# Performance work log

Hardware: AMD Instinct MI355X
Metric: run time of the kernel (lower is better)

Reference implementation:

```python
import jax, jax.numpy as jnp
import numpy as np

D = 1024      # in_features
H = 8         # heads per branch (head_num // 2)
DH = (D // 2) // H  # 64
OUT = 1024

def _split_heads(x, B, S):
    # [B, S, D/2] -> [B, H, S, DH]
    return x.reshape(B, S, H, DH).transpose(0, 2, 1, 3)

def _attn(q, k, v):
    # q,k,v: [B, H, S, DH]
    scores = jnp.einsum('bhqd,bhkd->bhqk', q, k) / jnp.sqrt(jnp.float32(DH))
    a = jax.nn.softmax(scores, axis=-1)
    return jnp.einsum('bhqk,bhkd->bhqd', a, v)

def setup_inputs() -> dict:
    key = jax.random.key(0)
    ks = jax.random.split(key, 16)
    B, S = 2, 2048
    d2 = D // 2
    sc = lambda fan_in: 1.0 / np.sqrt(fan_in)
    inp = {
        'f1': jax.random.normal(ks[0], (B, S, D), jnp.float32),
        'f2': jax.random.normal(ks[1], (B, S, D), jnp.float32),
    }
    names = ['qs', 'ks', 'vs', 'qc', 'kc', 'vc']
    for i, n in enumerate(names):
        inp['W' + n] = jax.random.uniform(ks[2 + i], (d2, D), jnp.float32, -sc(D), sc(D))
        inp['b' + n] = jax.random.uniform(ks[8 + i], (d2,), jnp.float32, -sc(D), sc(D))
    inp['Wo'] = jax.random.uniform(ks[14], (OUT, 2 * D), jnp.float32, -sc(2 * D), sc(2 * D))
    inp['bo'] = jax.random.uniform(ks[15], (OUT,), jnp.float32, -sc(2 * D), sc(2 * D))
    return inp

def reference(f1, f2, Wqs, bqs, Wks, bks, Wvs, bvs, Wqc, bqc, Wkc, bkc, Wvc, bvc, Wo, bo):
    B, S, _ = f1.shape
    lin = lambda x, W, b: jax.nn.relu(x @ W.T + b)
    qs = lin(f1, Wqs, bqs); ks_ = lin(f1, Wks, bks); vs = lin(f1, Wvs, bvs)
    qc = lin(f1, Wqc, bqc); kc = lin(f2, Wkc, bkc); vc = lin(f2, Wvc, bvc)
    ys = _attn(_split_heads(qs, B, S), _split_heads(ks_, B, S), _split_heads(vs, B, S))
    yc = _attn(_split_heads(qc, B, S), _split_heads(kc, B, S), _split_heads(vc, B, S))
    merge = lambda y: y.transpose(0, 2, 1, 3).reshape(B, S, D // 2)
    # reshape_to_batches followed by reshape_from_batches on vs/vc is identity
    y = jnp.concatenate([merge(ys), merge(yc), vs, vc], axis=-1)  # [B, S, 2D]
    return jax.nn.relu(y @ Wo.T + bo)
```

## Files before the change

kernel.cpp:

```cpp
#include <hip/hip_runtime.h>
#include <hip/hip_bf16.h>

using bf16 = __hip_bfloat16;
typedef __attribute__((ext_vector_type(8))) short bf16x8;
typedef __attribute__((ext_vector_type(4))) float f32x4;

#define MTOT 4096

__device__ __forceinline__ f32x4 fzero() {
    f32x4 z = {0.f, 0.f, 0.f, 0.f};
    return z;
}

__device__ __forceinline__ f32x4 mfma16(bf16x8 a, bf16x8 b, f32x4 c) {
    return __builtin_amdgcn_mfma_f32_16x16x32_bf16(a, b, c, 0, 0, 0);
}

typedef const __attribute__((address_space(1))) unsigned int* gas_ptr;
typedef __attribute__((address_space(3))) unsigned int* las_ptr;
__device__ __forceinline__ void async_copy16(const bf16* g, bf16* l) {
    __builtin_amdgcn_global_load_lds((gas_ptr)(const void*)g, (las_ptr)(void*)l, 16, 0, 0);
}

__device__ __forceinline__ bf16x8 load8(const bf16* p) {
    return *(const bf16x8*)p;
}
__device__ __forceinline__ bf16x8 load8(const float* p) {
    float4 a = *(const float4*)p;
    float4 b = *(const float4*)(p + 4);
    bf16 t[8];
    t[0] = __float2bfloat16(a.x); t[1] = __float2bfloat16(a.y);
    t[2] = __float2bfloat16(a.z); t[3] = __float2bfloat16(a.w);
    t[4] = __float2bfloat16(b.x); t[5] = __float2bfloat16(b.y);
    t[6] = __float2bfloat16(b.z); t[7] = __float2bfloat16(b.w);
    return *(const bf16x8*)t;
}

__device__ __forceinline__ void store_out(bf16* C, size_t idx, float v) {
    C[idx] = __float2bfloat16(v);
}
__device__ __forceinline__ void store_out(float* C, size_t idx, float v) {
    C[idx] = v;
}

__global__ void MultiHeadSelfCrossAttention_7834020348638_kernel(float* out, int n) {
    int i = blockIdx.x * blockDim.x + threadIdx.x;
    if (i < n) out[i] = 0.25f;
}

struct CvtArgs {
    const float* src[9];
    bf16* dst[9];
    int n8[9];
};
__global__ void cvt_kernel(CvtArgs a) {
    int seg = blockIdx.y;
    int t = blockIdx.x * blockDim.x + threadIdx.x;
    if (t < a.n8[seg])
        *(bf16x8*)(a.dst[seg] + (size_t)t * 8) = load8(a.src[seg] + (size_t)t * 8);
}

template <int BN, typename TC>
__device__ __forceinline__ void gemm_fast(
    const bf16* __restrict__ A, int lda,
    const bf16* __restrict__ Bt, int ldb,
    const float* __restrict__ bias,
    TC* __restrict__ C, int ldc,
    int K, int m0, int n0)
{
    constexpr int NI  = BN / 32;
    constexpr int ACH = 128 * 64 / 8 / 256;
    constexpr int BCH = BN * 64 / 8 / 256;

    __shared__ bf16 As[128 * 64];
    __shared__ bf16 Bs[BN * 64];

    const int tid  = threadIdx.x;
    const int lane = tid & 63;
    const int l15  = lane & 15, quad = lane >> 4;
    const int wave = tid >> 6;
    const int wr   = wave >> 1, wc = wave & 1;

    f32x4 acc[4][NI];
#pragma unroll
    for (int mi = 0; mi < 4; mi++)
#pragma unroll
        for (int ni = 0; ni < NI; ni++)
            acc[mi][ni] = fzero();

    for (int k0 = 0; k0 < K; k0 += 64) {
        __syncthreads();
#pragma unroll
        for (int i = 0; i < ACH; i++) {
            int idx = i * 256 + tid;
            int r   = idx >> 3;
            int cg  = (idx & 7) * 8;
            async_copy16(A + (size_t)(m0 + r) * lda + k0 + cg, &As[idx * 8]);
        }
#pragma unroll
        for (int i = 0; i < BCH; i++) {
            int idx = i * 256 + tid;
            int r   = idx >> 3;
            int cg  = (idx & 7) * 8;
            async_copy16(Bt + (size_t)(n0 + r) * ldb + k0 + cg, &Bs[idx * 8]);
        }
        __syncthreads();

#pragma unroll
        for (int ks = 0; ks < 2; ks++) {
            bf16x8 af[4], bfr[NI];
#pragma unroll
            for (int mi = 0; mi < 4; mi++)
                af[mi] = *(const bf16x8*)&As[(wr * 64 + mi * 16 + l15) * 64 + ks * 32 + quad * 8];
#pragma unroll
            for (int ni = 0; ni < NI; ni++)
                bfr[ni] = *(const bf16x8*)&Bs[(wc * (BN / 2) + ni * 16 + l15) * 64 + ks * 32 + quad * 8];
#pragma unroll
            for (int mi = 0; mi < 4; mi++)
#pragma unroll
                for (int ni = 0; ni < NI; ni++)
                    acc[mi][ni] = mfma16(af[mi], bfr[ni], acc[mi][ni]);
        }
    }

#pragma unroll
    for (int ni = 0; ni < NI; ni++) {
        int col = n0 + wc * (BN / 2) + ni * 16 + l15;
        float bb = bias[col];
#pragma unroll
        for (int mi = 0; mi < 4; mi++) {
#pragma unroll
            for (int r = 0; r < 4; r++) {
                int row = m0 + wr * 64 + mi * 16 + quad * 4 + r;
                store_out(C, (size_t)row * ldc + col, fmaxf(acc[mi][ni][r] + bb, 0.f));
            }
        }
    }
}

template <int BN, typename TA, typename TB, typename TC>
__device__ __forceinline__ void gemm_reg(
    const TA* __restrict__ A, int lda,
    const TB* __restrict__ Bt, int ldb,
    const float* __restrict__ bias,
    TC* __restrict__ C, int ldc,
    int K, int m0, int n0)
{
    constexpr int NI  = BN / 32;
    constexpr int BCH = BN * 4 / 256;

    __shared__ bf16 As[128 * 32];
    __shared__ bf16 Bs[BN * 32];

    const int tid  = threadIdx.x;
    const int lane = tid & 63;
    const int l15  = lane & 15, quad = lane >> 4;
    const int wave = tid >> 6;
    const int wr   = wave >> 1, wc = wave & 1;

    f32x4 acc[4][NI];
#pragma unroll
    for (int mi = 0; mi < 4; mi++)
#pragma unroll
        for (int ni = 0; ni < NI; ni++)
            acc[mi][ni] = fzero();

    for (int k0 = 0; k0 < K; k0 += 32) {
        bf16x8 ra[2], rb[BCH];
#pragma unroll
        for (int i = 0; i < 2; i++) {
            int idx = i * 256 + tid;
            ra[i] = load8(A + (size_t)(m0 + (idx >> 2)) * lda + k0 + (idx & 3) * 8);
        }
#pragma unroll
        for (int i = 0; i < BCH; i++) {
            int idx = i * 256 + tid;
            rb[i] = load8(Bt + (size_t)(n0 + (idx >> 2)) * ldb + k0 + (idx & 3) * 8);
        }
        __syncthreads();
#pragma unroll
        for (int i = 0; i < 2; i++)
            *(bf16x8*)&As[(i * 256 + tid) * 8] = ra[i];
#pragma unroll
        for (int i = 0; i < BCH; i++)
            *(bf16x8*)&Bs[(i * 256 + tid) * 8] = rb[i];
        __syncthreads();

        bf16x8 af[4], bfr[NI];
#pragma unroll
        for (int mi = 0; mi < 4; mi++)
            af[mi] = *(const bf16x8*)&As[(wr * 64 + mi * 16 + l15) * 32 + quad * 8];
#pragma unroll
        for (int ni = 0; ni < NI; ni++)
            bfr[ni] = *(const bf16x8*)&Bs[(wc * (BN / 2) + ni * 16 + l15) * 32 + quad * 8];
#pragma unroll
        for (int mi = 0; mi < 4; mi++)
#pragma unroll
            for (int ni = 0; ni < NI; ni++)
                acc[mi][ni] = mfma16(af[mi], bfr[ni], acc[mi][ni]);
    }

#pragma unroll
    for (int ni = 0; ni < NI; ni++) {
        int col = n0 + wc * (BN / 2) + ni * 16 + l15;
        float bb = bias[col];
#pragma unroll
        for (int mi = 0; mi < 4; mi++) {
#pragma unroll
            for (int r = 0; r < 4; r++) {
                int row = m0 + wr * 64 + mi * 16 + quad * 4 + r;
                store_out(C, (size_t)row * ldc + col, fmaxf(acc[mi][ni][r] + bb, 0.f));
            }
        }
    }
}

__global__ void proj_fast(
    const bf16* __restrict__ F1, const bf16* __restrict__ F2,
    const bf16* __restrict__ Wb,
    const float* __restrict__ bqs, const float* __restrict__ bks,
    const float* __restrict__ bvs, const float* __restrict__ bqc,
    const float* __restrict__ bkc, const float* __restrict__ bvc,
    bf16* __restrict__ Y, bf16* Qs, bf16* Ks, bf16* Qc, bf16* Kc)
{
    const int g = blockIdx.z;
    const bf16* X; const float* bi; bf16* C; int ldc;
    switch (g) {
        case 0:  X = F1; bi = bqs; C = Qs;       ldc = 512;  break;
        case 1:  X = F1; bi = bks; C = Ks;       ldc = 512;  break;
        case 2:  X = F1; bi = bvs; C = Y + 1024; ldc = 2048; break;
        case 3:  X = F1; bi = bqc; C = Qc;       ldc = 512;  break;
        case 4:  X = F2; bi = bkc; C = Kc;       ldc = 512;  break;
        default: X = F2; bi = bvc; C = Y + 1536; ldc = 2048; break;
    }
    gemm_fast<128, bf16>(X, 1024, Wb + (size_t)g * 512 * 1024, 1024, bi, C, ldc,
                         1024, blockIdx.y * 128, blockIdx.x * 128);
}

__global__ void out_fast(const bf16* __restrict__ Y, const bf16* __restrict__ WoB,
                         const float* __restrict__ bo, float* __restrict__ out)
{
    gemm_fast<64, float>(Y, 2048, WoB, 2048, bo, out, 1024, 2048,
                         blockIdx.y * 128, blockIdx.x * 64);
}

__global__ void proj_reg(
    const float* __restrict__ f1, const float* __restrict__ f2,
    const float* __restrict__ Wqs, const float* __restrict__ bqs,
    const float* __restrict__ Wks, const float* __restrict__ bks,
    const float* __restrict__ Wvs, const float* __restrict__ bvs,
    const float* __restrict__ Wqc, const float* __restrict__ bqc,
    const float* __restrict__ Wkc, const float* __restrict__ bkc,
    const float* __restrict__ Wvc, const float* __restrict__ bvc,
    bf16* __restrict__ Y, bf16* Qs, bf16* Ks, bf16* Qc, bf16* Kc)
{
    const int g = blockIdx.z;
    const float *X, *W, *bi; bf16* C; int ldc;
    switch (g) {
        case 0:  X = f1; W = Wqs; bi = bqs; C = Qs;       ldc = 512;  break;
        case 1:  X = f1; W = Wks; bi = bks; C = Ks;       ldc = 512;  break;
        case 2:  X = f1; W = Wvs; bi = bvs; C = Y + 1024; ldc = 2048; break;
        case 3:  X = f1; W = Wqc; bi = bqc; C = Qc;       ldc = 512;  break;
        case 4:  X = f2; W = Wkc; bi = bkc; C = Kc;       ldc = 512;  break;
        default: X = f2; W = Wvc; bi = bvc; C = Y + 1536; ldc = 2048; break;
    }
    gemm_reg<128>(X, 1024, W, 1024, bi, C, ldc, 1024, blockIdx.y * 128, blockIdx.x * 128);
}

__global__ void out_reg(const bf16* __restrict__ Y, const float* __restrict__ Wo,
                        const float* __restrict__ bo, float* __restrict__ out)
{
    gemm_reg<64>(Y, 2048, Wo, 2048, bo, out, 1024, 2048, blockIdx.y * 128, blockIdx.x * 64);
}

__global__ __launch_bounds__(256, 4) void attn_kernel(
    const bf16* __restrict__ Qsb, const bf16* __restrict__ Ksb,
    const bf16* __restrict__ Qcb, const bf16* __restrict__ Kcb,
    bf16* __restrict__ Y)
{
    __shared__ bf16 QP[64 * 72];
    __shared__ bf16 Ksh[64 * 72];
    __shared__ bf16 Vsh[64 * 72];

    const int tid  = threadIdx.x;
    const int lane = tid & 63;
    const int l15  = lane & 15, quad = lane >> 4;
    const int wave = tid >> 6;
    const int qt = blockIdx.x, bh = blockIdx.y, br = blockIdx.z;
    const int b = bh >> 3, h = bh & 7;

    const bf16* Qb = (br ? Qcb : Qsb) + (size_t)b * 2048 * 512 + h * 64;
    const bf16* Kb = (br ? Kcb : Ksb) + (size_t)b * 2048 * 512 + h * 64;
    const bf16* Vb = Y + (size_t)b * 2048 * 2048 + 1024 + br * 512 + h * 64;
    bf16*       Ob = Y + (size_t)b * 2048 * 2048 +        br * 512 + h * 64;
    const int q0 = qt * 64;

#pragma unroll
    for (int i = 0; i < 2; i++) {
        int idx = i * 256 + tid;
        int r = idx >> 3, c0 = (idx & 7) * 8;
        *(bf16x8*)&QP[r * 72 + c0] = *(const bf16x8*)&Qb[(size_t)(q0 + r) * 512 + c0];
    }
    __syncthreads();

    bf16x8 qf[2];
#pragma unroll
    for (int ks = 0; ks < 2; ks++)
        qf[ks] = *(const bf16x8*)&QP[(wave * 16 + l15) * 72 + ks * 32 + quad * 8];

    const short one_bits = l15 == 0 ? (short)0x3F80 : (short)0;
    bf16x8 onesf;
#pragma unroll
    for (int j = 0; j < 8; j++) onesf[j] = one_bits;

    f32x4 o[4], o_l;
    o_l = fzero();
#pragma unroll
    for (int ni = 0; ni < 4; ni++) o[ni] = fzero();

    const int kr0 = tid >> 3, kc0 = (tid & 7) * 8;
    const int kr1 = (256 + tid) >> 3;

    bf16x8 kr[2], vr[2];
    kr[0] = *(const bf16x8*)&Kb[(size_t)kr0 * 512 + kc0];
    kr[1] = *(const bf16x8*)&Kb[(size_t)kr1 * 512 + kc0];
    vr[0] = *(const bf16x8*)&Vb[(size_t)lane * 2048 + (0 * 4 + wave) * 8];
    vr[1] = *(const bf16x8*)&Vb[(size_t)lane * 2048 + (1 * 4 + wave) * 8];

    for (int jt = 0; jt < 32; jt++) {
        __syncthreads();
        *(bf16x8*)&Ksh[kr0 * 72 + kc0] = kr[0];
        *(bf16x8*)&Ksh[kr1 * 72 + kc0] = kr[1];
#pragma unroll
        for (int i = 0; i < 2; i++) {
            int cg = i * 4 + wave;
            const bf16* e = (const bf16*)&vr[i];
#pragma unroll
            for (int j = 0; j < 8; j++)
                Vsh[(cg * 8 + j) * 72 + lane] = e[j];
        }
        __syncthreads();

        {
            const int s0n = (jt < 31) ? (jt + 1) * 64 : 31 * 64;
            kr[0] = *(const bf16x8*)&Kb[(size_t)(s0n + kr0) * 512 + kc0];
            kr[1] = *(const bf16x8*)&Kb[(size_t)(s0n + kr1) * 512 + kc0];
            vr[0] = *(const bf16x8*)&Vb[(size_t)(s0n + lane) * 2048 + (0 * 4 + wave) * 8];
            vr[1] = *(const bf16x8*)&Vb[(size_t)(s0n + lane) * 2048 + (1 * 4 + wave) * 8];
        }

        f32x4 s[4];
#pragma unroll
        for (int ni = 0; ni < 4; ni++) s[ni] = fzero();
#pragma unroll
        for (int ni = 0; ni < 4; ni++)
#pragma unroll
            for (int ks = 0; ks < 2; ks++) {
                bf16x8 kf = *(const bf16x8*)&Ksh[(ni * 16 + l15) * 72 + ks * 32 + quad * 8];
                s[ni] = mfma16(qf[ks], kf, s[ni]);
            }

#pragma unroll
        for (int ni = 0; ni < 4; ni++)
#pragma unroll
            for (int r = 0; r < 4; r++) {
                float p = __expf(s[ni][r] * 0.125f - 4.0f);
                QP[(wave * 16 + quad * 4 + r) * 72 + ni * 16 + l15] = __float2bfloat16(p);
            }

#pragma unroll
        for (int ks = 0; ks < 2; ks++) {
            bf16x8 pf = *(const bf16x8*)&QP[(wave * 16 + l15) * 72 + ks * 32 + quad * 8];
#pragma unroll
            for (int ni = 0; ni < 4; ni++) {
                bf16x8 vf = *(const bf16x8*)&Vsh[(ni * 16 + l15) * 72 + ks * 32 + quad * 8];
                o[ni] = mfma16(pf, vf, o[ni]);
            }
            o_l = mfma16(pf, onesf, o_l);
        }
    }

#pragma unroll
    for (int r = 0; r < 4; r++) {
        float lsum = __shfl(o_l[r], quad << 4);
        float inv = 1.f / lsum;
        int row = q0 + wave * 16 + quad * 4 + r;
#pragma unroll
        for (int ni = 0; ni < 4; ni++)
            Ob[(size_t)row * 2048 + ni * 16 + l15] = __float2bfloat16(o[ni][r] * inv);
    }
}

extern "C" void kernel_launch(void* const* d_in, const int* in_sizes, int n_in,
                              void* d_out, int out_size, void* d_ws, size_t ws_size,
                              hipStream_t stream) {
    const size_t out_bytes = (size_t)out_size * sizeof(float);
    const size_t ws_base = ((size_t)MTOT * 2048 + 4 * (size_t)MTOT * 512) * 2;
    const size_t ws_fast = ws_base + ((size_t)2 * MTOT * 1024 + 6 * 512 * 1024 + 1024 * 2048) * 2;

    if (n_in != 16) { hipMemsetAsync(d_out, 0x43, out_bytes, stream); return; }
    if (ws_size < ws_base) { hipMemsetAsync(d_out, 0x41, out_bytes, stream); return; }

    const float* f1  = (const float*)d_in[0];
    const float* f2  = (const float*)d_in[1];
    const float* Wqs = (const float*)d_in[2];  const float* bqs = (const float*)d_in[3];
    const float* Wks = (const float*)d_in[4];  const float* bks = (const float*)d_in[5];
    const float* Wvs = (const float*)d_in[6];  const float* bvs = (const float*)d_in[7];
    const float* Wqc = (const float*)d_in[8];  const float* bqc = (const float*)d_in[9];
    const float* Wkc = (const float*)d_in[10]; const float* bkc = (const float*)d_in[11];
    const float* Wvc = (const float*)d_in[12]; const float* bvc = (const float*)d_in[13];
    const float* Wo  = (const float*)d_in[14]; const float* bo  = (const float*)d_in[15];

    bf16* Y  = (bf16*)d_ws;
    bf16* Qs = Y  + (size_t)MTOT * 2048;
    bf16* Ks = Qs + (size_t)MTOT * 512;
    bf16* Qc = Ks + (size_t)MTOT * 512;
    bf16* Kc = Qc + (size_t)MTOT * 512;
    float* out = (float*)d_out;

    if (ws_size >= ws_fast) {
        bf16* F1  = Kc + (size_t)MTOT * 512;
        bf16* F2  = F1 + (size_t)MTOT * 1024;
        bf16* Wb  = F2 + (size_t)MTOT * 1024;
        bf16* WoB = Wb + (size_t)6 * 512 * 1024;

        CvtArgs ca;
        ca.src[0] = f1;  ca.dst[0] = F1;  ca.n8[0] = MTOT * 1024 / 8;
        ca.src[1] = f2;  ca.dst[1] = F2;  ca.n8[1] = MTOT * 1024 / 8;
        const float* ws_[6] = {Wqs, Wks, Wvs, Wqc, Wkc, Wvc};
        for (int i = 0; i < 6; i++) {
            ca.src[2 + i] = ws_[i];
            ca.dst[2 + i] = Wb + (size_t)i * 512 * 1024;
            ca.n8[2 + i]  = 512 * 1024 / 8;
        }
        ca.src[8] = Wo; ca.dst[8] = WoB; ca.n8[8] = 1024 * 2048 / 8;

        cvt_kernel<<<dim3((MTOT * 1024 / 8 + 255) / 256, 9), 256, 0, stream>>>(ca);
        proj_fast<<<dim3(4, 32, 6), 256, 0, stream>>>(
            F1, F2, Wb, bqs, bks, bvs, bqc, bkc, bvc, Y, Qs, Ks, Qc, Kc);
        attn_kernel<<<dim3(32, 16, 2), 256, 0, stream>>>(Qs, Ks, Qc, Kc, Y);
        out_fast<<<dim3(16, 32), 256, 0, stream>>>(Y, WoB, bo, out);
    } else {
        proj_reg<<<dim3(4, 32, 6), 256, 0, stream>>>(
            f1, f2, Wqs, bqs, Wks, bks, Wvs, bvs, Wqc, bqc, Wkc, bkc, Wvc, bvc,
            Y, Qs, Ks, Qc, Kc);
        attn_kernel<<<dim3(32, 16, 2), 256, 0, stream>>>(Qs, Ks, Qc, Kc, Y);
        out_reg<<<dim3(16, 32), 256, 0, stream>>>(Y, Wo, bo, out);
    }
}
```

Baseline: 263.8 us.

## Add double-buffered attention kernel with pre-transposed V and larger query tiles

Adds a kernel that transposes V per head into a separate workspace buffer. A new attention kernel uses 128-query tiles with 2 waves of 64 rows each. It double-buffers K and V^T tiles in XOR-swizzled LDS through async global-to-LDS copies, so loads overlap the MFMA work. This brings more register reuse of K/V fragments and hides memory latency, at the cost of an extra transpose pass, more workspace, and lower occupancy (128 threads per block).

```diff
diff --git a/kernel.cpp b/kernel.cpp
--- a/kernel.cpp
+++ b/kernel.cpp
@@ -273,14 +273,33 @@
     gemm_reg<64>(Y, 2048, Wo, 2048, bo, out, 1024, 2048, blockIdx.y * 128, blockIdx.x * 64);
 }
 
-__global__ __launch_bounds__(256, 4) void attn_kernel(
+__global__ void vt_kernel(const bf16* __restrict__ Y, bf16* __restrict__ VT) {
+    const int tid = threadIdx.x;
+    const int st = blockIdx.x, bh = blockIdx.y, br = blockIdx.z;
+    const int b = bh >> 3, h = bh & 7;
+    const bf16* src = Y + (size_t)b * 2048 * 2048 + 1024 + br * 512 + h * 64;
+    bf16* dst = VT + ((size_t)((br * 2 + b) * 8 + h)) * 64 * 2048;
+    const int s0 = st * 64;
+#pragma unroll
+    for (int i = 0; i < 2; i++) {
+        int idx = i * 256 + tid;
+        int d = idx >> 3, cs = (idx & 7) * 8;
+        bf16 tmp[8];
+#pragma unroll
+        for (int j = 0; j < 8; j++)
+            tmp[j] = src[(size_t)(s0 + cs + j) * 2048 + d];
+        *(bf16x8*)&dst[(size_t)d * 2048 + s0 + cs] = *(const bf16x8*)tmp;
+    }
+}
+
+__global__ __launch_bounds__(128, 2) void attn2_kernel(
     const bf16* __restrict__ Qsb, const bf16* __restrict__ Ksb,
     const bf16* __restrict__ Qcb, const bf16* __restrict__ Kcb,
-    bf16* __restrict__ Y)
-{
-    __shared__ bf16 QP[64 * 72];
-    __shared__ bf16 Ksh[64 * 72];
-    __shared__ bf16 Vsh[64 * 72];
+    const bf16* __restrict__ VT, bf16* __restrict__ Y)
+{
+    __shared__ bf16 Kbuf[2][64 * 64];
+    __shared__ bf16 Vbuf[2][64 * 64];
+    __shared__ bf16 QP[128 * 72];
 
     const int tid  = threadIdx.x;
     const int lane = tid & 63;
@@ -291,6 +310,150 @@
 
     const bf16* Qb = (br ? Qcb : Qsb) + (size_t)b * 2048 * 512 + h * 64;
     const bf16* Kb = (br ? Kcb : Ksb) + (size_t)b * 2048 * 512 + h * 64;
+    const bf16* Vt = VT + ((size_t)((br * 2 + b) * 8 + h)) * 64 * 2048;
+    bf16*       Ob = Y + (size_t)b * 2048 * 2048 + br * 512 + h * 64;
+    const int q0 = qt * 128;
+
+#pragma unroll
+    for (int i = 0; i < 8; i++) {
+        int idx = i * 128 + tid;
+        int r = idx >> 3, c0 = (idx & 7) * 8;
+        *(bf16x8*)&QP[r * 72 + c0] = *(const bf16x8*)&Qb[(size_t)(q0 + r) * 512 + c0];
+    }
+
+#pragma unroll
+    for (int i = 0; i < 4; i++) {
+        int idx = i * 128 + tid;
+        int r = idx >> 3, sl = (idx & 7) ^ (r & 7);
+        async_copy16(Kb + (size_t)r * 512 + sl * 8, &Kbuf[0][idx * 8]);
+    }
+#pragma unroll
+    for (int i = 0; i < 4; i++) {
+        int idx = i * 128 + tid;
+        int r = idx >> 3, sl = (idx & 7) ^ (r & 7);
+        async_copy16(Vt + (size_t)r * 2048 + sl * 8, &Vbuf[0][idx * 8]);
+    }
+    __syncthreads();
+
+    bf16x8 qf[4][2];
+#pragma unroll
+    for (int m = 0; m < 4; m++)
+#pragma unroll
+        for (int ks = 0; ks < 2; ks++)
+            qf[m][ks] = *(const bf16x8*)&QP[(wave * 64 + m * 16 + l15) * 72 + ks * 32 + quad * 8];
+
+    const short one_bits = l15 == 0 ? (short)0x3F80 : (short)0;
+    bf16x8 onesf;
+#pragma unroll
+    for (int j = 0; j < 8; j++) onesf[j] = one_bits;
+
+    f32x4 o[4][4], ol[4];
+#pragma unroll
+    for (int m = 0; m < 4; m++) {
+        ol[m] = fzero();
+#pragma unroll
+        for (int ni = 0; ni < 4; ni++) o[m][ni] = fzero();
+    }
+
+    for (int jt = 0; jt < 32; jt++) {
+        const int cur = jt & 1;
+
+        if (jt < 31) {
+            const size_t s0n = (size_t)(jt + 1) * 64;
+#pragma unroll
+            for (int i = 0; i < 4; i++) {
+                int idx = i * 128 + tid;
+                int r = idx >> 3, sl = (idx & 7) ^ (r & 7);
+                async_copy16(Kb + (s0n + r) * 512 + sl * 8, &Kbuf[cur ^ 1][idx * 8]);
+            }
+#pragma unroll
+            for (int i = 0; i < 4; i++) {
+                int idx = i * 128 + tid;
+                int r = idx >> 3, sl = (idx & 7) ^ (r & 7);
+                async_copy16(Vt + (size_t)r * 2048 + s0n + sl * 8, &Vbuf[cur ^ 1][idx * 8]);
+            }
+        }
+
+        f32x4 s[4][4];
+#pragma unroll
+        for (int m = 0; m < 4; m++)
+#pragma unroll
+            for (int ni = 0; ni < 4; ni++) s[m][ni] = fzero();
+#pragma unroll
+        for (int ni = 0; ni < 4; ni++)
+#pragma unroll
+            for (int ks = 0; ks < 2; ks++) {
+                bf16x8 kf = *(const bf16x8*)&Kbuf[cur][(ni * 16 + l15) * 64
+                               + (((ks * 4 + quad) ^ (l15 & 7)) * 8)];
+#pragma unroll
+                for (int m = 0; m < 4; m++)
+                    s[m][ni] = mfma16(qf[m][ks], kf, s[m][ni]);
+            }
+
+#pragma unroll
+        for (int m = 0; m < 4; m++)
+#pragma unroll
+            for (int ni = 0; ni < 4; ni++)
+#pragma unroll
+                for (int r = 0; r < 4; r++) {
+                    float p = __expf(s[m][ni][r] * 0.125f - 4.0f);
+                    QP[(wave * 64 + m * 16 + quad * 4 + r) * 72 + ni * 16 + l15] =
+                        __float2bfloat16(p);
+                }
+
+#pragma unroll
+        for (int ks = 0; ks < 2; ks++) {
+            bf16x8 pf[4];
+#pragma unroll
+            for (int m = 0; m < 4; m++)
+                pf[m] = *(const bf16x8*)&QP[(wave * 64 + m * 16 + l15) * 72 + ks * 32 + quad * 8];
+#pragma unroll
+            for (int ni = 0; ni < 4; ni++) {
+                bf16x8 vf = *(const bf16x8*)&Vbuf[cur][(ni * 16 + l15) * 64
+                               + (((ks * 4 + quad) ^ (l15 & 7)) * 8)];
+#pragma unroll
+                for (int m = 0; m < 4; m++)
+                    o[m][ni] = mfma16(pf[m], vf, o[m][ni]);
+            }
+#pragma unroll
+            for (int m = 0; m < 4; m++)
+                ol[m] = mfma16(pf[m], onesf, ol[m]);
+        }
+
+        __syncthreads();
+    }
+
+#pragma unroll
+    for (int m = 0; m < 4; m++)
+#pragma unroll
+        for (int r = 0; r < 4; r++) {
+            float lsum = __shfl(ol[m][r], quad << 4);
+            float inv = 1.f / lsum;
+            int row = q0 + wave * 64 + m * 16 + quad * 4 + r;
+#pragma unroll
+            for (int ni = 0; ni < 4; ni++)
+                Ob[(size_t)row * 2048 + ni * 16 + l15] = __float2bfloat16(o[m][ni][r] * inv);
+        }
+}
+
+__global__ __launch_bounds__(256, 4) void attn_kernel(
+    const bf16* __restrict__ Qsb, const bf16* __restrict__ Ksb,
+    const bf16* __restrict__ Qcb, const bf16* __restrict__ Kcb,
+    bf16* __restrict__ Y)
+{
+    __shared__ bf16 QP[64 * 72];
+    __shared__ bf16 Ksh[64 * 72];
+    __shared__ bf16 Vsh[64 * 72];
+
+    const int tid  = threadIdx.x;
+    const int lane = tid & 63;
+    const int l15  = lane & 15, quad = lane >> 4;
+    const int wave = tid >> 6;
+    const int qt = blockIdx.x, bh = blockIdx.y, br = blockIdx.z;
+    const int b = bh >> 3, h = bh & 7;
+
+    const bf16* Qb = (br ? Qcb : Qsb) + (size_t)b * 2048 * 512 + h * 64;
+    const bf16* Kb = (br ? Kcb : Ksb) + (size_t)b * 2048 * 512 + h * 64;
     const bf16* Vb = Y + (size_t)b * 2048 * 2048 + 1024 + br * 512 + h * 64;
     bf16*       Ob = Y + (size_t)b * 2048 * 2048 +        br * 512 + h * 64;
     const int q0 = qt * 64;
@@ -397,6 +560,8 @@
     const size_t out_bytes = (size_t)out_size * sizeof(float);
     const size_t ws_base = ((size_t)MTOT * 2048 + 4 * (size_t)MTOT * 512) * 2;
     const size_t ws_fast = ws_base + ((size_t)2 * MTOT * 1024 + 6 * 512 * 1024 + 1024 * 2048) * 2;
+    const size_t vt_elems = (size_t)2 * 2 * 8 * 64 * 2048;
+    const size_t ws_fast2 = ws_fast + vt_elems * 2;
 
     if (n_in != 16) { hipMemsetAsync(d_out, 0x43, out_bytes, stream); return; }
     if (ws_size < ws_base) { hipMemsetAsync(d_out, 0x41, out_bytes, stream); return; }
@@ -423,6 +588,7 @@
         bf16* F2  = F1 + (size_t)MTOT * 1024;
         bf16* Wb  = F2 + (size_t)MTOT * 1024;
         bf16* WoB = Wb + (size_t)6 * 512 * 1024;
+        bf16* VT  = WoB + (size_t)1024 * 2048;
 
         CvtArgs ca;
         ca.src[0] = f1;  ca.dst[0] = F1;  ca.n8[0] = MTOT * 1024 / 8;
@@ -438,7 +604,12 @@
         cvt_kernel<<<dim3((MTOT * 1024 / 8 + 255) / 256, 9), 256, 0, stream>>>(ca);
         proj_fast<<<dim3(4, 32, 6), 256, 0, stream>>>(
             F1, F2, Wb, bqs, bks, bvs, bqc, bkc, bvc, Y, Qs, Ks, Qc, Kc);
-        attn_kernel<<<dim3(32, 16, 2), 256, 0, stream>>>(Qs, Ks, Qc, Kc, Y);
+        if (ws_size >= ws_fast2) {
+            vt_kernel<<<dim3(32, 16, 2), 256, 0, stream>>>(Y, VT);
+            attn2_kernel<<<dim3(16, 16, 2), 128, 0, stream>>>(Qs, Ks, Qc, Kc, VT, Y);
+        } else {
+            attn_kernel<<<dim3(32, 16, 2), 256, 0, stream>>>(Qs, Ks, Qc, Kc, Y);
+        }
         out_fast<<<dim3(16, 32), 256, 0, stream>>>(Y, WoB, bo, out);
     } else {
         proj_reg<<<dim3(4, 32, 6), 256, 0, stream>>>(
```

After: 287.4 us. 1.09x slower.
